# Kernel tuning notes

Measured on AMD Instinct MI355X. Metric: run time of the kernel, lower is better.

Reference implementation:

```python
import jax, jax.numpy as jnp
import numpy as np

NUM_SAMPLES = 512
FG_FRAC = 0.25
BATCH = 64
N = 131072


def _subsample(key, indicator, labels):
    """Faithful port of BalancedPositiveNegativeSampler._static_subsample.

    indicator: bool [N] sample candidates; labels: bool [N] positive flags.
    Returns int32 [N] indicator of sampled examples (1 = sampled).
    """
    n = indicator.shape[0]
    # Pad indicator with extra False examples so at least NUM_SAMPLES are True.
    num_true = jnp.sum(indicator.astype(jnp.float32))
    additional_false = jnp.cumsum((~indicator).astype(jnp.float32)) <= (NUM_SAMPLES - num_true)
    ind = indicator | additional_false
    # Random shuffle (permutation stored to restore order post-sampling).
    perm = jax.random.permutation(key, n)
    ind_p = ind[perm]
    lab_p = labels[perm]
    # 1-based index where indicator True, 0 otherwise; sign by label.
    idx = jnp.where(ind_p, jnp.arange(1, n + 1, dtype=jnp.int32), jnp.int32(0))
    signed = jnp.where(lab_p, jnp.int32(1), jnp.int32(-1))
    s_idx = idx * signed
    # Descending sort: positives first, then zeros, then negatives (most-negative last).
    sorted_desc = jnp.flip(jnp.sort(s_idx))
    # Balanced pos/neg counts.
    num_pos_avail = jnp.sum((sorted_desc > 0).astype(jnp.int32))
    max_pos = jnp.int32(int(NUM_SAMPLES * FG_FRAC))
    num_pos = jnp.minimum(max_pos, num_pos_avail)
    # Take first num_pos from the start and (NUM_SAMPLES - num_pos) from the end.
    rk = jnp.arange(NUM_SAMPLES, dtype=jnp.int32)
    gather_idx = jnp.where(rk < num_pos, rk, n - NUM_SAMPLES + rk)
    sampled = sorted_desc[gather_idx]
    # Back to 0-based indices; clamp empty slots to 0.
    sampled = jnp.abs(sampled) - 1
    sampled = jnp.where(sampled >= 0, sampled, 0)
    # Indicator in shuffled order, then scatter back through the permutation.
    ind2 = jnp.zeros(n, jnp.int32).at[sampled].set(1)
    out = jnp.zeros(n, jnp.int32).at[perm].set(ind2)
    return out


def setup_inputs() -> dict:
    key = jax.random.key(0)
    k1, k2, k3 = jax.random.split(key, 3)
    positive_matches = jax.random.bernoulli(k1, 0.01, (BATCH, N))
    negative_matches = jax.random.bernoulli(k2, 0.70, (BATCH, N)) & (~positive_matches)
    ignored_matches = jax.random.bernoulli(k3, 0.05, (BATCH, N)) & (~positive_matches) & (~negative_matches)
    return {
        "positive_matches": positive_matches,
        "negative_matches": negative_matches,
        "ignored_matches": ignored_matches,
    }


def reference(positive_matches, negative_matches, ignored_matches):
    b = positive_matches.shape[0]
    candidates = (positive_matches | negative_matches) & (~ignored_matches)
    keys = jax.random.split(jax.random.key(42), b)
    sampled_indicators = jax.vmap(_subsample)(keys, candidates, positive_matches)  # int32 [B, N]
    # Final top_k over {0,1} indicators: selected indices first (ascending), then rest.
    _, selected_indices = jax.lax.top_k(sampled_indicators, NUM_SAMPLES)
    return selected_indices
```

## Files before the change

kernel.cpp:

```cpp
#include <hip/hip_runtime.h>
#include <stdint.h>

#define BATCH 64
#define NN 131072
#define NCOARSE 256
#define SLOT 704
#define CHUNK 4096
#define NSUB 1024
#define EMASK17 0x1FFFFu
#define POSCAP 1536
#define NEGCAP 1536
#define SPOSCAP 96
#define SNEGCAP 160

typedef uint32_t u32;
typedef uint64_t u64;

__device__ __forceinline__ u32 rotl32(u32 v, int d) { return (v << d) | (v >> (32 - d)); }

__device__ __forceinline__ void threefry2x32(u32 k0, u32 k1, u32 x0, u32 x1, u32& o0, u32& o1) {
  u32 ks2 = k0 ^ k1 ^ 0x1BD11BDAu;
  x0 += k0; x1 += k1;
#define TF_R(r) { x0 += x1; x1 = rotl32(x1, r); x1 ^= x0; }
  TF_R(13) TF_R(15) TF_R(26) TF_R(6)
  x0 += k1;  x1 += ks2 + 1u;
  TF_R(17) TF_R(29) TF_R(16) TF_R(24)
  x0 += ks2; x1 += k0 + 2u;
  TF_R(13) TF_R(15) TF_R(26) TF_R(6)
  x0 += k0;  x1 += k1 + 3u;
  TF_R(17) TF_R(29) TF_R(16) TF_R(24)
  x0 += k1;  x1 += ks2 + 4u;
  TF_R(13) TF_R(15) TF_R(26) TF_R(6)
  x0 += ks2; x1 += k0 + 5u;
#undef TF_R
  o0 = x0; o1 = x1;
}

__device__ __forceinline__ u32 tf_bits(u32 k0, u32 k1, u32 i) {
  u32 o0, o1;
  threefry2x32(k0, k1, 0u, i, o0, o1);
  return o0 ^ o1;
}

__device__ void batch_round_key(int b, int round, u32& rk0, u32& rk1) {
  u32 kb0, kb1;
  threefry2x32(0u, 42u, 0u, (u32)b, kb0, kb1);
  if (round == 1) { threefry2x32(kb0, kb1, 0u, 1u, rk0, rk1); return; }
  u32 c0, c1;
  threefry2x32(kb0, kb1, 0u, 0u, c0, c1);
  threefry2x32(c0, c1, 0u, 1u, rk0, rk1);
}


__global__ __launch_bounds__(512) void scatterA_kernel(u32* __restrict__ cursor, u32* __restrict__ meta,
                                                       u64* __restrict__ binned,
                                                       const int* __restrict__ posg, const int* __restrict__ negg,
                                                       const int* __restrict__ igng, int batch0) {
  __shared__ u32 sk[2];
  __shared__ u32 hist[NCOARSE];
  __shared__ u32 lstart[NCOARSE];
  __shared__ u32 gbase[NCOARSE];
  __shared__ u64 staged[CHUNK];
  __shared__ u32 wtot4[4];
  __shared__ u32 cntPN[2];
  int g = blockIdx.y;
  int b = batch0 + g;
  int tid = threadIdx.x;
  if (tid == 0) { u32 k0, k1; batch_round_key(b, 1, k0, k1); sk[0] = k0; sk[1] = k1; }
  if (tid < 2) cntPN[tid] = 0;
  if (tid < NCOARSE) hist[tid] = 0;
  __syncthreads();
  u32 base = blockIdx.x * CHUNK;
  u64 recs[8]; u32 rr[8];
  u32 myp = 0, myn = 0;
  const int4* P4 = (const int4*)(posg + (size_t)b * NN);
  const int4* Q4 = (const int4*)(negg + (size_t)b * NN);
  const int4* I4 = (const int4*)(igng + (size_t)b * NN);
#pragma unroll
  for (int j = 0; j < 2; j++) {
    u32 e0 = base + j * 2048 + tid * 4;
    int4 pv = P4[e0 >> 2];
    int4 nv = Q4[e0 >> 2];
    int4 iv = I4[e0 >> 2];
#pragma unroll
    for (int m = 0; m < 4; m++) {
      u32 e = e0 + m;
      int p = (&pv.x)[m] != 0, n = (&nv.x)[m] != 0, ig = (&iv.x)[m] != 0;
      u32 label = ((p | n) && !ig) ? (p ? 1u : 2u) : 0u;
      myp += (label == 1);
      myn += (label == 2);
      u32 k1 = tf_bits(sk[0], sk[1], e);
      u32 bin = k1 >> 24;
      rr[j * 4 + m] = atomicAdd(&hist[bin], 1u);
      recs[j * 4 + m] = ((u64)k1 << 19) | ((u64)e << 2) | (u64)label;
    }
  }
#pragma unroll
  for (int off = 32; off > 0; off >>= 1) {
    myp += __shfl_down(myp, off, 64);
    myn += __shfl_down(myn, off, 64);
  }
  if ((tid & 63) == 0) { atomicAdd(&cntPN[0], myp); atomicAdd(&cntPN[1], myn); }
  __syncthreads();
  u32 hv = 0, hs = 0;
  if (tid < NCOARSE) {
    hv = hist[tid];
    hs = hv;
#pragma unroll
    for (int off = 1; off < 64; off <<= 1) {
      u32 t = __shfl_up(hs, off, 64);
      if ((tid & 63) >= off) hs += t;
    }
    if ((tid & 63) == 63) wtot4[tid >> 6] = hs;
  }
  __syncthreads();
  if (tid < NCOARSE) {
    u32 woff = 0;
    for (int w = 0; w < (tid >> 6); w++) woff += wtot4[w];
    lstart[tid] = hs + woff - hv;
  }
  __syncthreads();
#pragma unroll
  for (int j = 0; j < 8; j++) {
    u32 bin = (u32)(recs[j] >> 43);
    staged[lstart[bin] + rr[j]] = recs[j];
  }
  if (tid < NCOARSE) {
    u32 c = hist[tid];
    gbase[tid] = c ? atomicAdd(&cursor[(size_t)g * NCOARSE + tid], c) : 0u;
  }
  __syncthreads();
  u64* bn = binned + (size_t)g * NCOARSE * SLOT;
  for (int s = tid; s < CHUNK; s += 512) {
    u64 v = staged[s];
    u32 bin = (u32)(v >> 43);
    u32 off = gbase[bin] + ((u32)s - lstart[bin]);
    if (off < SLOT) bn[(size_t)bin * SLOT + off] = v;
  }
  __syncthreads();
  if (tid < 2) atomicAdd(&meta[(size_t)g * 16 + 2 + tid], cntPN[tid]);
}

__global__ __launch_bounds__(256) void passB_kernel(const u32* __restrict__ cursor,
                                                    const u64* __restrict__ binned,
                                                    u32* __restrict__ meta,
                                                    u64* __restrict__ posbuf, u64* __restrict__ negbuf,
                                                    int batch0) {
  __shared__ u32 sk2[2];
  __shared__ u32 sth[2];
  __shared__ u64 keys[SLOT];
  __shared__ u32 hist[NSUB];
  __shared__ u32 sstart[NSUB];
  __shared__ u32 wtot[4];
  __shared__ u32 bstart[NCOARSE];
  __shared__ u32 bcnt[NCOARSE];
  __shared__ u64 sposb[SPOSCAP];
  __shared__ u64 snegb[SNEGCAP];
  __shared__ u32 lcb[2], lbase[2];
  int g = blockIdx.y;
  int tid = threadIdx.x;
  if (tid == 0) {
    u32 a, c;
    batch_round_key(batch0 + g, 2, a, c); sk2[0] = a; sk2[1] = c;
    lcb[0] = 0; lcb[1] = 0;
    u32 np = meta[(size_t)g * 16 + 2], nn = meta[(size_t)g * 16 + 3];
    u32 qp = np < 128 ? np : 128;
    u32 qn = 512 - qp;
    u32 needp = qp + 96, needn = qn + 160;
    u32 tp = 0, tn = 0;
    if (np > needp) { u32 d = (256u * needp + np - 1) / np; if (d < 256) tp = 256 - d; }
    if (nn > needn) { u32 d = (256u * needn + nn - 1) / nn; if (d < 256) tn = 256 - d; }
    sth[0] = tp; sth[1] = tn;
  }
  {
    u32 bv = cursor[(size_t)g * NCOARSE + tid];
    u32 bs = bv;
#pragma unroll
    for (int off = 1; off < 64; off <<= 1) {
      u32 t2 = __shfl_up(bs, off, 64);
      if ((tid & 63) >= off) bs += t2;
    }
    if ((tid & 63) == 63) wtot[tid >> 6] = bs;
    __syncthreads();
    u32 woff = 0;
    for (int w = 0; w < (tid >> 6); w++) woff += wtot[w];
    bstart[tid] = bs + woff - bv;
    bcnt[tid] = bv;
  }
  __syncthreads();
  const u64* bn = binned + (size_t)g * NCOARSE * SLOT;
  u32 tp = sth[0], tn = sth[1];
  for (int q = 0; q < 8; q++) {
    u32 bin = blockIdx.x * 8 + q;
    u32 cb = bcnt[bin];
    if (cb > SLOT) cb = SLOT;
    u32 start = bstart[bin];
    hist[tid] = 0; hist[tid + 256] = 0; hist[tid + 512] = 0; hist[tid + 768] = 0;
    __syncthreads();
    u64 mykey[3]; u32 mysr[3];
#pragma unroll
    for (int t = 0; t < 3; t++) {
      int i = tid + t * 256;
      if (i < (int)cb) {
        u64 key = bn[(size_t)bin * SLOT + i];
        u32 sub = (u32)(key >> 33) & 0x3FFu;
        u32 r = atomicAdd(&hist[sub], 1u);
        mykey[t] = key;
        mysr[t] = (sub << 10) | r;
      } else {
        mysr[t] = 0xFFFFFFFFu;
      }
    }
    __syncthreads();
    u32 h0 = hist[4 * tid], h1 = hist[4 * tid + 1], h2 = hist[4 * tid + 2], h3 = hist[4 * tid + 3];
    u32 s = h0 + h1 + h2 + h3;
    u32 v = s;
#pragma unroll
    for (int off = 1; off < 64; off <<= 1) {
      u32 t2 = __shfl_up(v, off, 64);
      if ((tid & 63) >= off) v += t2;
    }
    if ((tid & 63) == 63) wtot[tid >> 6] = v;
    __syncthreads();
    u32 woff = 0;
    for (int w = 0; w < (tid >> 6); w++) woff += wtot[w];
    u32 excl = v + woff - s;
    sstart[4 * tid] = excl;
    sstart[4 * tid + 1] = excl + h0;
    sstart[4 * tid + 2] = excl + h0 + h1;
    sstart[4 * tid + 3] = excl + h0 + h1 + h2;
    __syncthreads();
#pragma unroll
    for (int t = 0; t < 3; t++) {
      if (mysr[t] != 0xFFFFFFFFu)
        keys[sstart[mysr[t] >> 10] + (mysr[t] & 0x3FFu)] = mykey[t];
    }
    __syncthreads();
#pragma unroll
    for (int t = 0; t < 3; t++) {
      int i = tid + t * 256;
      if (i < (int)cb) {
        u64 ki = keys[i];
        u32 sub = (u32)(ki >> 33) & 0x3FFu;
        u32 s0 = sstart[sub], h = hist[sub];
        u32 r = 0;
        for (u32 j = s0; j < s0 + h; j++) {
          if (keys[j] < ki) r++;
        }
        u32 p1 = start + s0 + r;
        u32 label = (u32)ki & 3u;
        if (label) {
          u32 e = (u32)(ki >> 2) & EMASK17;
          u32 k2 = tf_bits(sk2[0], sk2[1], p1);
          u32 b8 = k2 >> 24;
          u64 rec = ((u64)p1 << 32) | e;
          if (label == 1) {
            if (b8 >= tp) {
              u32 rr2 = atomicAdd(&lcb[0], 1u);
              if (rr2 < SPOSCAP) sposb[rr2] = rec;
              else {
                u32 s2 = atomicAdd(&meta[(size_t)g * 16], 1u);
                if (s2 < POSCAP) posbuf[(size_t)g * POSCAP + s2] = rec;
              }
            }
          } else {
            if (b8 >= tn) {
              u32 rr2 = atomicAdd(&lcb[1], 1u);
              if (rr2 < SNEGCAP) snegb[rr2] = rec;
              else {
                u32 s2 = atomicAdd(&meta[(size_t)g * 16 + 1], 1u);
                if (s2 < NEGCAP) negbuf[(size_t)g * NEGCAP + s2] = rec;
              }
            }
          }
        }
      }
    }
    __syncthreads();
  }
  if (tid < 2) {
    u32 n = lcb[tid]; u32 cap = tid ? SNEGCAP : SPOSCAP; if (n > cap) n = cap;
    lbase[tid] = n ? atomicAdd(&meta[(size_t)g * 16 + tid], n) : 0u;
  }
  __syncthreads();
  {
    u32 n0 = lcb[0]; if (n0 > SPOSCAP) n0 = SPOSCAP;
    for (u32 i = tid; i < n0; i += 256) {
      u32 s2 = lbase[0] + i;
      if (s2 < POSCAP) posbuf[(size_t)g * POSCAP + s2] = sposb[i];
    }
    u32 n1 = lcb[1]; if (n1 > SNEGCAP) n1 = SNEGCAP;
    for (u32 i = tid; i < n1; i += 256) {
      u32 s2 = lbase[1] + i;
      if (s2 < NEGCAP) negbuf[(size_t)g * NEGCAP + s2] = snegb[i];
    }
  }
}

__global__ __launch_bounds__(1024) void select_final_kernel(const u32* __restrict__ meta,
                                                            const u64* __restrict__ posbuf,
                                                            const u64* __restrict__ negbuf,
                                                            int* __restrict__ out, int batch0) {
  int g = blockIdx.x, tid = threadIdx.x, b = batch0 + g;
  __shared__ u32 sk2[2];
  __shared__ u64 keyP[POSCAP + 8];
  __shared__ u32 valP[POSCAP];
  __shared__ u64 keyN[NEGCAP + 8];
  __shared__ u32 valN[NEGCAP];
  __shared__ int sel[512];
  if (tid == 0) { u32 a, c; batch_round_key(b, 2, a, c); sk2[0] = a; sk2[1] = c; }
  u32 np = meta[(size_t)g * 16 + 2];
  u32 qp = np < 128 ? np : 128;
  u32 qn = 512 - qp;
  u32 cp = meta[(size_t)g * 16]; if (cp > POSCAP) cp = POSCAP;
  u32 cn = meta[(size_t)g * 16 + 1]; if (cn > NEGCAP) cn = NEGCAP;
  u32 cp8 = (cp + 7) & ~7u;
  u32 cn8 = (cn + 7) & ~7u;
  if (tid < 512) sel[tid] = 0;
  __syncthreads();

  if (tid < 512) {
    for (u32 i = tid; i < cp8; i += 512) {
      if (i < cp) {
        u64 rec = posbuf[(size_t)g * POSCAP + i];
        u32 p1 = (u32)(rec >> 32);
        keyP[i] = ((u64)tf_bits(sk2[0], sk2[1], p1) << 32) | p1;
        valP[i] = (u32)rec;
      } else {
        keyP[i] = 0ull;
      }
    }
  } else {
    u32 t2 = tid - 512;
    for (u32 i = t2; i < cn8; i += 512) {
      if (i < cn) {
        u64 rec = negbuf[(size_t)g * NEGCAP + i];
        u32 p1 = (u32)(rec >> 32);
        keyN[i] = ((u64)tf_bits(sk2[0], sk2[1], p1) << 32) | p1;
        valN[i] = (u32)rec;
      } else {
        keyN[i] = 0ull;
      }
    }
  }
  __syncthreads();

  if (tid < 512) {
#pragma unroll
    for (int t = 0; t < 3; t++) {
      u32 i = tid + t * 512;
      if (i < cp) {
        u64 mk = keyP[i];
        u32 r = 0;
        for (u32 j = 0; j < cp8; j += 8) {
          r += (keyP[j] > mk) + (keyP[j + 1] > mk) + (keyP[j + 2] > mk) + (keyP[j + 3] > mk) +
               (keyP[j + 4] > mk) + (keyP[j + 5] > mk) + (keyP[j + 6] > mk) + (keyP[j + 7] > mk);
        }
        if (r < qp) sel[r] = (int)valP[i];
      }
    }
  } else {
    u32 t2 = tid - 512;
#pragma unroll
    for (int t = 0; t < 3; t++) {
      u32 i = t2 + t * 512;
      if (i < cn) {
        u64 mk = keyN[i];
        u32 r = 0;
        for (u32 j = 0; j < cn8; j += 8) {
          r += (keyN[j] > mk) + (keyN[j + 1] > mk) + (keyN[j + 2] > mk) + (keyN[j + 3] > mk) +
               (keyN[j + 4] > mk) + (keyN[j + 5] > mk) + (keyN[j + 6] > mk) + (keyN[j + 7] > mk);
        }
        if (r < qn) sel[qp + r] = (int)valN[i];
      }
    }
  }
  __syncthreads();

  if (tid < 512) {
    int v = sel[tid];
    u32 r = 0;
    for (int j = 0; j < 512; j += 8) {
      r += (sel[j] < v) + (sel[j + 1] < v) + (sel[j + 2] < v) + (sel[j + 3] < v) +
           (sel[j + 4] < v) + (sel[j + 5] < v) + (sel[j + 6] < v) + (sel[j + 7] < v);
    }
    out[(size_t)b * 512 + r] = v;
  }
}

extern "C" void kernel_launch(void* const* d_in, const int* in_sizes, int n_in,
                              void* d_out, int out_size, void* d_ws, size_t ws_size,
                              hipStream_t stream) {
  const int* pos = (const int*)d_in[0];
  const int* neg = (const int*)d_in[1];
  const int* ign = (const int*)d_in[2];
  int* out = (int*)d_out;

  size_t perBatch = (NCOARSE + 16) * 4 + (size_t)NCOARSE * SLOT * 8 +
                    (size_t)POSCAP * 8 + (size_t)NEGCAP * 8;
  int G = (int)(ws_size / perBatch);
  if (G > BATCH) G = BATCH;
  if (G < 1) G = 1;

  char* p = (char*)d_ws;
  u32* cursor = (u32*)p;            p += (size_t)G * NCOARSE * 4;
  u32* meta = (u32*)p;              p += (size_t)G * 16 * 4;
  size_t zeroBytes = (size_t)p - (size_t)d_ws;
  u64* binned = (u64*)p;            p += (size_t)G * NCOARSE * SLOT * 8;
  u64* posbuf = (u64*)p;            p += (size_t)G * POSCAP * 8;
  u64* negbuf = (u64*)p;            p += (size_t)G * NEGCAP * 8;

  for (int batch0 = 0; batch0 < BATCH; batch0 += G) {
    int Gi = (BATCH - batch0 < G) ? (BATCH - batch0) : G;
    hipMemsetAsync(d_ws, 0, zeroBytes, stream);
    dim3 gridS(NN / CHUNK, Gi);
    scatterA_kernel<<<gridS, 512, 0, stream>>>(cursor, meta, binned, pos, neg, ign, batch0);
    dim3 gridP(NCOARSE / 8, Gi);
    passB_kernel<<<gridP, 256, 0, stream>>>(cursor, binned, meta, posbuf, negbuf, batch0);
    select_final_kernel<<<Gi, 1024, 0, stream>>>(meta, posbuf, negbuf, out, batch0);
  }
}
```

Before: 217.9 us.

## Compress binned records to 32-bit and recompute hash in second pass

The scatter pass now stores 32-bit tokens (element index plus label) instead of 64-bit keys holding the full random hash. The second pass recomputes the threefry hash for each binned element, trading extra ALU work for half the binned-buffer traffic and smaller shared staging. The chunk per block is also doubled to 8192 elements with 16 records per thread, which halves the block count and raises register pressure.

```diff
diff --git a/kernel.cpp b/kernel.cpp
--- a/kernel.cpp
+++ b/kernel.cpp
@@ -5,7 +5,7 @@
 #define NN 131072
 #define NCOARSE 256
 #define SLOT 704
-#define CHUNK 4096
+#define CHUNK 8192
 #define NSUB 1024
 #define EMASK17 0x1FFFFu
 #define POSCAP 1536
@@ -53,14 +53,14 @@
 
 
 __global__ __launch_bounds__(512) void scatterA_kernel(u32* __restrict__ cursor, u32* __restrict__ meta,
-                                                       u64* __restrict__ binned,
+                                                       u32* __restrict__ binned,
                                                        const int* __restrict__ posg, const int* __restrict__ negg,
                                                        const int* __restrict__ igng, int batch0) {
   __shared__ u32 sk[2];
   __shared__ u32 hist[NCOARSE];
   __shared__ u32 lstart[NCOARSE];
   __shared__ u32 gbase[NCOARSE];
-  __shared__ u64 staged[CHUNK];
+  __shared__ u32 staged[CHUNK];
   __shared__ u32 wtot4[4];
   __shared__ u32 cntPN[2];
   int g = blockIdx.y;
@@ -71,13 +71,13 @@
   if (tid < NCOARSE) hist[tid] = 0;
   __syncthreads();
   u32 base = blockIdx.x * CHUNK;
-  u64 recs[8]; u32 rr[8];
+  u32 recs[16]; u32 rr[16];
   u32 myp = 0, myn = 0;
   const int4* P4 = (const int4*)(posg + (size_t)b * NN);
   const int4* Q4 = (const int4*)(negg + (size_t)b * NN);
   const int4* I4 = (const int4*)(igng + (size_t)b * NN);
 #pragma unroll
-  for (int j = 0; j < 2; j++) {
+  for (int j = 0; j < 4; j++) {
     u32 e0 = base + j * 2048 + tid * 4;
     int4 pv = P4[e0 >> 2];
     int4 nv = Q4[e0 >> 2];
@@ -92,7 +92,7 @@
       u32 k1 = tf_bits(sk[0], sk[1], e);
       u32 bin = k1 >> 24;
       rr[j * 4 + m] = atomicAdd(&hist[bin], 1u);
-      recs[j * 4 + m] = ((u64)k1 << 19) | ((u64)e << 2) | (u64)label;
+      recs[j * 4 + m] = (bin << 24) | (label << 17) | e;
     }
   }
 #pragma unroll
@@ -121,8 +121,8 @@
   }
   __syncthreads();
 #pragma unroll
-  for (int j = 0; j < 8; j++) {
-    u32 bin = (u32)(recs[j] >> 43);
+  for (int j = 0; j < 16; j++) {
+    u32 bin = recs[j] >> 24;
     staged[lstart[bin] + rr[j]] = recs[j];
   }
   if (tid < NCOARSE) {
@@ -130,23 +130,23 @@
     gbase[tid] = c ? atomicAdd(&cursor[(size_t)g * NCOARSE + tid], c) : 0u;
   }
   __syncthreads();
-  u64* bn = binned + (size_t)g * NCOARSE * SLOT;
+  u32* bn = binned + (size_t)g * NCOARSE * SLOT;
   for (int s = tid; s < CHUNK; s += 512) {
-    u64 v = staged[s];
-    u32 bin = (u32)(v >> 43);
+    u32 v = staged[s];
+    u32 bin = v >> 24;
     u32 off = gbase[bin] + ((u32)s - lstart[bin]);
-    if (off < SLOT) bn[(size_t)bin * SLOT + off] = v;
+    if (off < SLOT) bn[(size_t)bin * SLOT + off] = v & 0x7FFFFu;
   }
   __syncthreads();
   if (tid < 2) atomicAdd(&meta[(size_t)g * 16 + 2 + tid], cntPN[tid]);
 }
 
 __global__ __launch_bounds__(256) void passB_kernel(const u32* __restrict__ cursor,
-                                                    const u64* __restrict__ binned,
+                                                    const u32* __restrict__ binned,
                                                     u32* __restrict__ meta,
                                                     u64* __restrict__ posbuf, u64* __restrict__ negbuf,
                                                     int batch0) {
-  __shared__ u32 sk2[2];
+  __shared__ u32 sk1[2], sk2[2];
   __shared__ u32 sth[2];
   __shared__ u64 keys[SLOT];
   __shared__ u32 hist[NSUB];
@@ -161,6 +161,7 @@
   int tid = threadIdx.x;
   if (tid == 0) {
     u32 a, c;
+    batch_round_key(batch0 + g, 1, a, c); sk1[0] = a; sk1[1] = c;
     batch_round_key(batch0 + g, 2, a, c); sk2[0] = a; sk2[1] = c;
     lcb[0] = 0; lcb[1] = 0;
     u32 np = meta[(size_t)g * 16 + 2], nn = meta[(size_t)g * 16 + 3];
@@ -188,7 +189,7 @@
     bcnt[tid] = bv;
   }
   __syncthreads();
-  const u64* bn = binned + (size_t)g * NCOARSE * SLOT;
+  const u32* bn = binned + (size_t)g * NCOARSE * SLOT;
   u32 tp = sth[0], tn = sth[1];
   for (int q = 0; q < 8; q++) {
     u32 bin = blockIdx.x * 8 + q;
@@ -202,7 +203,11 @@
     for (int t = 0; t < 3; t++) {
       int i = tid + t * 256;
       if (i < (int)cb) {
-        u64 key = bn[(size_t)bin * SLOT + i];
+        u32 tok = bn[(size_t)bin * SLOT + i];
+        u32 e = tok & EMASK17;
+        u32 label = tok >> 17;
+        u32 k1 = tf_bits(sk1[0], sk1[1], e);
+        u64 key = ((u64)k1 << 19) | ((u64)e << 2) | (u64)label;
         u32 sub = (u32)(key >> 33) & 0x3FFu;
         u32 r = atomicAdd(&hist[sub], 1u);
         mykey[t] = key;
@@ -396,7 +401,7 @@
   const int* ign = (const int*)d_in[2];
   int* out = (int*)d_out;
 
-  size_t perBatch = (NCOARSE + 16) * 4 + (size_t)NCOARSE * SLOT * 8 +
+  size_t perBatch = (NCOARSE + 16) * 4 + (size_t)NCOARSE * SLOT * 4 +
                     (size_t)POSCAP * 8 + (size_t)NEGCAP * 8;
   int G = (int)(ws_size / perBatch);
   if (G > BATCH) G = BATCH;
@@ -406,7 +411,7 @@
   u32* cursor = (u32*)p;            p += (size_t)G * NCOARSE * 4;
   u32* meta = (u32*)p;              p += (size_t)G * 16 * 4;
   size_t zeroBytes = (size_t)p - (size_t)d_ws;
-  u64* binned = (u64*)p;            p += (size_t)G * NCOARSE * SLOT * 8;
+  u32* binned = (u32*)p;            p += (size_t)G * NCOARSE * SLOT * 4;
   u64* posbuf = (u64*)p;            p += (size_t)G * POSCAP * 8;
   u64* negbuf = (u64*)p;            p += (size_t)G * NEGCAP * 8;
 
```

Result: slower. 225.9 us (+3.7%).
